# Performance work log

Hardware: AMD Instinct MI355X
Metric: run time of the kernel (lower is better)

The kernel has to match this reference:

```python
import jax, jax.numpy as jnp
import numpy as np

B, T, D, R = 8, 2048, 2048, 4


def setup_inputs() -> dict:
    key = jax.random.key(0)
    ks = jax.random.split(key, 9)
    u = jax.random.normal(ks[0], (B, T, D), dtype=jnp.float32)
    # a chosen so tanh(a) ~ 0.995: keeps cumprod over T=2048 away from underflow
    a = 3.0 + 0.2 * jax.random.uniform(ks[1], (D,), dtype=jnp.float32)
    b = 0.02 * jax.random.normal(ks[2], (D,), dtype=jnp.float32)
    c = 0.02 * jax.random.normal(ks[3], (D,), dtype=jnp.float32)
    d = 0.02 * jax.random.normal(ks[4], (D,), dtype=jnp.float32)
    gate_w = jax.random.normal(ks[5], (D, D), dtype=jnp.float32) / np.float32(np.sqrt(D))
    gate_b = jnp.zeros((D,), dtype=jnp.float32)
    d_lr_u = 0.02 * jax.random.normal(ks[6], (D, R), dtype=jnp.float32)
    d_lr_v = 0.02 * jax.random.normal(ks[7], (R, D), dtype=jnp.float32)
    return {"u": u, "a": a, "b": b, "c": c, "d": d,
            "gate_w": gate_w, "gate_b": gate_b,
            "d_lr_u": d_lr_u, "d_lr_v": d_lr_v}


def reference(u, a, b, c, d, gate_w, gate_b, d_lr_u, d_lr_v):
    # u: [B,T,D]
    Bs, Ts, Ds = u.shape
    rank = d_lr_u.shape[1]
    # gated input (torch Linear: x @ W.T + bias)
    g = jax.nn.sigmoid(jnp.einsum('btd,ed->bte', u, gate_w) + gate_b)
    u_g = u * g
    aa = jnp.tanh(a)                                   # [D], in (-1,1)
    # low-rank correction to feedthrough d
    u_mean = jnp.mean(u_g, axis=1, keepdims=True)      # [B,1,D]
    d_lr = (u_mean @ d_lr_u) @ d_lr_v / max(1.0, float(rank))
    d_eff = d + d_lr                                   # [B,1,D]
    # diagonal SSM via cumprod/cumsum (G[t] = aa^(t+1)); per-channel, T-independent of B
    G = jnp.cumprod(jnp.broadcast_to(aa, (Ts, Ds)), axis=0)  # [T,D]
    bu = b * u_g                                       # [B,T,D]
    G_safe = G.at[0].set(jnp.maximum(G[0], 1e-6))
    z = bu / G_safe                                    # [B,T,D]
    s = G * jnp.cumsum(z, axis=1)                      # [B,T,D]
    y = c * s + d_eff * u_g
    return y
```

## Files before the change

kernel.cpp:

```cpp
#include <hip/hip_runtime.h>
#include <hip/hip_bf16.h>
#include <math.h>

#define Bq 8
#define Tq 2048
#define Dq 2048
#define Rq 4
#define Mq (Bq*Tq)
#define NC 16
#define CL (Tq/NC)

typedef __attribute__((ext_vector_type(8))) short bf16x8;
typedef __attribute__((ext_vector_type(4))) float f32x4;
typedef __attribute__((ext_vector_type(4))) unsigned short us4;
typedef __attribute__((ext_vector_type(8))) unsigned short us8;

__device__ __forceinline__ unsigned short f2bf(float x) {
    unsigned int u = __float_as_uint(x);
    unsigned int r = (u + 0x7fffu + ((u >> 16) & 1u)) >> 16;
    return (unsigned short)r;
}
__device__ __forceinline__ float bf2f(unsigned short h) {
    return __uint_as_float((unsigned)h << 16);
}

template<int UGBF>
__device__ __forceinline__ f32x4 ld4(const void* p, long long off) {
    if constexpr (UGBF) {
        us4 v = *(const us4*)((const unsigned short*)p + off);
        f32x4 r;
        r.x = bf2f(v.x); r.y = bf2f(v.y); r.z = bf2f(v.z); r.w = bf2f(v.w);
        return r;
    } else {
        return *(const f32x4*)((const float*)p + off);
    }
}

__global__ __launch_bounds__(256) void k0_convert(
    const float* __restrict__ u, const float* __restrict__ gw,
    const float* __restrict__ a,
    unsigned short* __restrict__ ubf, unsigned short* __restrict__ wbf,
    float* __restrict__ aat, float* __restrict__ aaLt,
    float* __restrict__ aapow)
{
    const long long uN4 = (long long)Mq * Dq / 4;
    const long long wN4 = (long long)Dq * Dq / 4;
    long long gid = (long long)blockIdx.x * blockDim.x + threadIdx.x;
    if (gid < Dq) {
        float aa = tanhf(a[gid]);
        aat[gid] = aa;
        aaLt[gid] = exp2f((float)CL * log2f(aa));
        float p = 1.0f;
        for (int k = 0; k <= 16; ++k) { aapow[k * Dq + gid] = p; p *= aa; }
    }
    long long stride = (long long)gridDim.x * blockDim.x;
    for (long long i = gid; i < uN4 + wN4; i += stride) {
        const float4* src; unsigned short* dst; long long j;
        if (i < uN4) { src = (const float4*)u;  dst = ubf; j = i; }
        else         { src = (const float4*)gw; dst = wbf; j = i - uN4; }
        float4 v = src[j];
        us4 p;
        p.x = f2bf(v.x); p.y = f2bf(v.y); p.z = f2bf(v.z); p.w = f2bf(v.w);
        *(us4*)(dst + j * 4) = p;
    }
}


#define PH_BAR __builtin_amdgcn_s_barrier()
#define PRIO1  __builtin_amdgcn_s_setprio(1)
#define PRIO0  __builtin_amdgcn_s_setprio(0)

#define LDA(K0, K1, qb) do { _Pragma("unroll") for (int f_ = 0; f_ < 4; ++f_) { \
    aF[0][f_] = *(const bf16x8*)&lds[(K0) + ((qb) + f_) * 1024]; \
    aF[1][f_] = *(const bf16x8*)&lds[(K1) + ((qb) + f_) * 1024]; } } while (0)

#define LDB(K0, K1, fnb) do { _Pragma("unroll") for (int f_ = 0; f_ < 2; ++f_) { \
    bF[0][(fnb) + f_] = *(const bf16x8*)&lds[(K0) + ((fnb) + f_) * 1024]; \
    bF[1][(fnb) + f_] = *(const bf16x8*)&lds[(K1) + ((fnb) + f_) * 1024]; } } while (0)

#define MMA(fmb, fnb) do { _Pragma("unroll") for (int ks_ = 0; ks_ < 2; ++ks_) \
    _Pragma("unroll") for (int fm_ = 0; fm_ < 4; ++fm_) \
    _Pragma("unroll") for (int fn_ = 0; fn_ < 2; ++fn_) \
        acc[(fmb) + fm_][(fnb) + fn_] = __builtin_amdgcn_mfma_f32_16x16x32_bf16( \
            aF[ks_][fm_], bF[ks_][(fnb) + fn_], acc[(fmb) + fm_][(fnb) + fn_], 0, 0, 0); } while (0)

#define GLD(P, DST) __builtin_amdgcn_global_load_lds( \
    (const __attribute__((address_space(1))) void*)(P), \
    (__attribute__((address_space(3))) void*)&lds[DST], 16, 0, 0)

#define STAGE4(P00, P01, P10, P11, DBASE, KOFF) do { \
    GLD((P00) + (KOFF), (DBASE));              \
    GLD((P01) + (KOFF), (DBASE) + 512);        \
    GLD((P10) + (KOFF), (DBASE) + 8192);       \
    GLD((P11) + (KOFF), (DBASE) + 8192 + 512); } while (0)

template<int UGBF>
__global__ __launch_bounds__(512, 2) void k1_gemm(
    const unsigned short* __restrict__ Abf,
    const unsigned short* __restrict__ Bbf,
    const float* __restrict__ gate_b,
    const float* __restrict__ bvec,
    const float* __restrict__ aapow,
    float* __restrict__ psum,
    float* __restrict__ carry,
    void* __restrict__ ug_)
{
    __shared__ unsigned short lds[65536];
    const int tid  = threadIdx.x;
    const int wave = tid >> 6, lane = tid & 63;
    const int wr = wave >> 2, wc = wave & 3;

    const int bid = blockIdx.x;
    const int swz = (bid & 7) * 64 + (bid >> 3);
    const int tm = (swz >> 3) * 256;
    const int tn = (swz & 7) * 256;

    const int rr = lane & 15, kq = lane >> 4;
    const int r7 = rr & 7;
    const int kb0 = (kq ^ r7) * 8;
    const int kb1 = ((4 + kq) ^ r7) * 8;

    const int aB = wr * 8192 + rr * 64;
    const int bB = 16384 + (wc >> 1) * 8192 + (wc & 1) * 4096 + rr * 64;
    const int swA0k0 = aB + kb0,          swA0k1 = aB + kb1;
    const int swA1k0 = aB + 32768 + kb0,  swA1k1 = aB + 32768 + kb1;
    const int swB0k0 = bB + kb0,          swB0k1 = bB + kb1;
    const int swB1k0 = bB + 32768 + kb0,  swB1k1 = bB + 32768 + kb1;

    const int grow  = lane >> 3;
    const int gslot = ((lane & 7) ^ grow) * 8;
    const unsigned short* gA00 = Abf + (long long)(tm + wave * 16 + grow) * Dq + gslot;
    const unsigned short* gA01 = gA00 + 8 * Dq;
    const unsigned short* gA10 = gA00 + 128 * Dq;
    const unsigned short* gA11 = gA00 + 136 * Dq;
    const unsigned short* gB00 = Bbf + (long long)(tn + wave * 16 + grow) * Dq + gslot;
    const unsigned short* gB01 = gB00 + 8 * Dq;
    const unsigned short* gB10 = gB00 + 128 * Dq;
    const unsigned short* gB11 = gB00 + 136 * Dq;

    f32x4 acc[8][4] = {};
    bf16x8 aF[2][4], bF[2][4];

    const int dA0 = wave * 1024;
    const int dB0 = 16384 + wave * 1024;

    STAGE4(gB00, gB01, gB10, gB11, dB0,         0);
    STAGE4(gA00, gA01, gA10, gA11, dA0,         0);
    STAGE4(gB00, gB01, gB10, gB11, dB0 + 32768, 64);
    STAGE4(gA00, gA01, gA10, gA11, dA0 + 32768, 64);
    asm volatile("s_waitcnt vmcnt(8)" ::: "memory");
    PH_BAR;

    const int NIT = Dq / 128;
    for (int it = 0; it < NIT; ++it) {
        const bool pre = (it < NIT - 1);

        LDA(swA0k0, swA0k1, 0); LDB(swB0k0, swB0k1, 0);
        PH_BAR; PRIO1; MMA(0, 0); PRIO0; PH_BAR;
        LDB(swB0k0, swB0k1, 2);
        PH_BAR; PRIO1; MMA(0, 2); PRIO0; PH_BAR;
        LDA(swA0k0, swA0k1, 4);
        if (pre) STAGE4(gB00, gB01, gB10, gB11, dB0, 128);
        PH_BAR; PRIO1; MMA(4, 0); PRIO0; PH_BAR;
        if (pre) STAGE4(gA00, gA01, gA10, gA11, dA0, 128);
        PH_BAR;
        if (pre) asm volatile("s_waitcnt vmcnt(8)" ::: "memory");
        else     asm volatile("s_waitcnt vmcnt(0)" ::: "memory");
        PRIO1; MMA(4, 2); PRIO0; PH_BAR;

        LDA(swA1k0, swA1k1, 0); LDB(swB1k0, swB1k1, 0);
        PH_BAR; PRIO1; MMA(0, 0); PRIO0; PH_BAR;
        LDB(swB1k0, swB1k1, 2);
        PH_BAR; PRIO1; MMA(0, 2); PRIO0; PH_BAR;
        LDA(swA1k0, swA1k1, 4);
        if (pre) STAGE4(gB00, gB01, gB10, gB11, dB0 + 32768, 192);
        PH_BAR; PRIO1; MMA(4, 0); PRIO0; PH_BAR;
        if (pre) STAGE4(gA00, gA01, gA10, gA11, dA0 + 32768, 192);
        PH_BAR;
        if (pre) asm volatile("s_waitcnt vmcnt(8)" ::: "memory");
        else     asm volatile("s_waitcnt vmcnt(0)" ::: "memory");
        PRIO1; MMA(4, 2); PRIO0; PH_BAR;

        gA00 += 128; gA01 += 128; gA10 += 128; gA11 += 128;
        gB00 += 128; gB01 += 128; gB10 += 128; gB11 += 128;
    }

#pragma unroll
    for (int fn = 0; fn < 4; ++fn) {
        const int col = wc * 64 + fn * 16 + rr;
        const float gb = gate_b[tn + col];
#pragma unroll
        for (int fm = 0; fm < 8; ++fm) {
#pragma unroll
            for (int j = 0; j < 4; ++j) {
                const int row = wr * 128 + fm * 16 + kq * 4 + j;
                const float logit = acc[fm][fn][j] + gb;
                const float sg = 1.0f / (1.0f + __expf(-logit));
                lds[row * 256 + (col ^ (kq << 4))] = f2bf(sg);
            }
        }
    }
    __syncthreads();

    const int lr2  = lane >> 5;
    const int cb32 = lane & 31;
    const int c0   = cb32 * 8;
    const int baseT = wave * 2 + lr2;
    const int cX = ((baseT >> 2) & 3) << 4;

    float bw[8], a16[8], w15[8];
    {
        const float* bp   = bvec + tn + c0;
        const float* a16p = aapow + 16 * Dq + tn + c0;
        const float* w15p = aapow + (15 - baseT) * Dq + tn + c0;
#pragma unroll
        for (int k = 0; k < 8; ++k) { bw[k] = bp[k]; a16[k] = a16p[k]; w15[k] = w15p[k]; }
    }

    float ps[2][8] = {}, cr[2][8] = {};
#pragma unroll
    for (int i = 0; i < 16; ++i) {
        const int r = baseT + i * 16;
        const int ck = i >> 3;
        const long long gidx = (long long)(tm + r) * Dq + tn + c0;
        const bf16x8 u8 = *(const bf16x8*)&Abf[gidx];
        const bf16x8 s8 = *(const bf16x8*)&lds[r * 256 + (c0 ^ cX)];
        float ug[8];
#pragma unroll
        for (int k = 0; k < 8; ++k) {
            ug[k] = bf2f((unsigned short)u8[k]) * bf2f((unsigned short)s8[k]);
            ps[ck][k] += ug[k];
            cr[ck][k] = a16[k] * cr[ck][k] + bw[k] * ug[k];
        }
        if constexpr (UGBF) {
            us8 o;
#pragma unroll
            for (int k = 0; k < 8; ++k) o[k] = f2bf(ug[k]);
            *(us8*)&((unsigned short*)ug_)[gidx] = o;
        } else {
            f32x4 o0, o1;
            o0.x = ug[0]; o0.y = ug[1]; o0.z = ug[2]; o0.w = ug[3];
            o1.x = ug[4]; o1.y = ug[5]; o1.z = ug[6]; o1.w = ug[7];
            *(f32x4*)&((float*)ug_)[gidx]     = o0;
            *(f32x4*)&((float*)ug_)[gidx + 4] = o1;
        }
    }
    __syncthreads();

    float* redf = (float*)lds;
    const int slot = (baseT + cb32) & 15;
#pragma unroll
    for (int ck = 0; ck < 2; ++ck)
#pragma unroll
        for (int k = 0; k < 8; ++k) {
            const int col = c0 + k;
            redf[((ck * 2 + 0) * 256 + col) * 16 + slot] = ps[ck][k];
            redf[((ck * 2 + 1) * 256 + col) * 16 + slot] = cr[ck][k] * w15[k];
        }
    __syncthreads();

    const int bb  = tm >> 11;
    const int ckb = (tm & 2047) >> 7;
#pragma unroll
    for (int ii = 0; ii < 2; ++ii) {
        const int item = tid + ii * 512;
        const int p = item >> 8, col = item & 255;
        const int ck = p >> 1, isC = p & 1;
        const int rot = (item & 3) * 4;
        float s = 0.f;
#pragma unroll
        for (int q = 0; q < 4; ++q) {
            const f32x4 v = *(const f32x4*)&redf[item * 16 + ((rot + q * 4) & 15)];
            s += v.x + v.y + v.z + v.w;
        }
        const long long gi = (long long)(bb * NC + ckb + ck) * Dq + tn + col;
        if (isC) carry[gi] = s; else psum[gi] = s;
    }
}

__global__ __launch_bounds__(256) void k3_deff(
    const float* __restrict__ psum, const float* __restrict__ dvec,
    const float* __restrict__ dlru, const float* __restrict__ dlrv,
    float* __restrict__ deff)
{
    const int bb = blockIdx.x, tid = threadIdx.x;
    __shared__ float red[4][256];
    __shared__ float proj[4];
    float pr[4] = {0.f, 0.f, 0.f, 0.f};
    for (int i = 0; i < Dq / 256; ++i) {
        int dd = tid + i * 256;
        float m = 0.f;
        for (int k = 0; k < NC; ++k) m += psum[((long long)bb * NC + k) * Dq + dd];
        m *= (1.0f / (float)Tq);
#pragma unroll
        for (int r = 0; r < 4; ++r) pr[r] += m * dlru[dd * Rq + r];
    }
#pragma unroll
    for (int r = 0; r < 4; ++r) red[r][tid] = pr[r];
    __syncthreads();
    for (int off = 128; off > 0; off >>= 1) {
        if (tid < off)
#pragma unroll
            for (int r = 0; r < 4; ++r) red[r][tid] += red[r][tid + off];
        __syncthreads();
    }
    if (tid < 4) proj[tid] = red[tid][0] * 0.25f;
    __syncthreads();
    float p0 = proj[0], p1 = proj[1], p2 = proj[2], p3 = proj[3];
    for (int i = 0; i < Dq / 256; ++i) {
        int e = tid + i * 256;
        float v = dvec[e] + p0 * dlrv[0 * Dq + e] + p1 * dlrv[1 * Dq + e]
                          + p2 * dlrv[2 * Dq + e] + p3 * dlrv[3 * Dq + e];
        deff[(long long)bb * Dq + e] = v;
    }
}

template<int UGBF>
__global__ __launch_bounds__(128) void k4_scanC(
    const void* __restrict__ ug, float* __restrict__ yout,
    const float* __restrict__ aat, const float* __restrict__ aaLt,
    const float* __restrict__ bvec, const float* __restrict__ cvec,
    const float* __restrict__ deff, const float* __restrict__ carry)
{
    const int d0 = blockIdx.x * 512 + threadIdx.x * 4;
    const int ck = blockIdx.y, bb = blockIdx.z;
    f32x4 aa  = *(const f32x4*)&aat[d0];
    f32x4 aaL = *(const f32x4*)&aaLt[d0];
    f32x4 bv  = *(const f32x4*)&bvec[d0];
    f32x4 cv  = *(const f32x4*)&cvec[d0];
    f32x4 de  = *(const f32x4*)&deff[(long long)bb * Dq + d0];
    f32x4 s = {0.f, 0.f, 0.f, 0.f};
    for (int j = 0; j < ck; ++j) {
        f32x4 cj = *(const f32x4*)&carry[((long long)bb * NC + j) * Dq + d0];
        s = aaL * s + cj;
    }
    const long long base = ((long long)bb * Tq + (long long)ck * CL) * Dq + d0;
    for (int t = 0; t < CL; ++t) {
        f32x4 x = ld4<UGBF>(ug, base + (long long)t * Dq);
        s = aa * s + bv * x;
        f32x4 y = cv * s + de * x;
        *(f32x4*)&yout[base + (long long)t * Dq] = y;
    }
}

extern "C" void kernel_launch(void* const* d_in, const int* in_sizes, int n_in,
                              void* d_out, int out_size, void* d_ws, size_t ws_size,
                              hipStream_t stream)
{
    const float* u    = (const float*)d_in[0];
    const float* a    = (const float*)d_in[1];
    const float* b    = (const float*)d_in[2];
    const float* c    = (const float*)d_in[3];
    const float* d    = (const float*)d_in[4];
    const float* gw   = (const float*)d_in[5];
    const float* gb   = (const float*)d_in[6];
    const float* dlru = (const float*)d_in[7];
    const float* dlrv = (const float*)d_in[8];
    float* out = (float*)d_out;

    char* ws = (char*)d_ws;
    const size_t sz_ubf = (size_t)Mq * Dq * 2;
    const size_t sz_wbf = (size_t)Dq * Dq * 2;
    const size_t sz_ug  = (size_t)Mq * Dq * 2;
    const size_t sz_ps  = (size_t)Bq * NC * Dq * 4;

    unsigned short* ubf = (unsigned short*)ws;
    unsigned short* wbf = (unsigned short*)(ws + sz_ubf);

    const size_t tail_sz = 2 * sz_ps + (size_t)Bq * Dq * 4
                         + 2 * (size_t)Dq * 4 + (size_t)17 * Dq * 4;
    const size_t need_bf16 = sz_ubf + sz_wbf + sz_ug + tail_sz;
    const bool ugbf_mode = (ws_size >= need_bf16);

    char* rest = ws + sz_ubf + sz_wbf;
    unsigned short* ugbf = (unsigned short*)rest;
    char* tail = ugbf_mode ? (rest + sz_ug) : rest;
    float* psum  = (float*)tail;
    float* carry = psum  + (size_t)Bq * NC * Dq;
    float* deff  = carry + (size_t)Bq * NC * Dq;
    float* aat   = deff  + (size_t)Bq * Dq;
    float* aaLt  = aat   + Dq;
    float* aapow = aaLt  + Dq;

    k0_convert<<<2048, 256, 0, stream>>>(u, gw, a, ubf, wbf, aat, aaLt, aapow);

    dim3 g2(Dq / 512, NC, Bq);
    if (ugbf_mode) {
        k1_gemm<1><<<512, 512, 0, stream>>>(ubf, wbf, gb, b, aapow, psum, carry, ugbf);
        k3_deff<<<Bq, 256, 0, stream>>>(psum, d, dlru, dlrv, deff);
        k4_scanC<1><<<g2, 128, 0, stream>>>(ugbf, out, aat, aaLt, b, c, deff, carry);
    } else {
        k1_gemm<0><<<512, 512, 0, stream>>>(ubf, wbf, gb, b, aapow, psum, carry, out);
        k3_deff<<<Bq, 256, 0, stream>>>(psum, d, dlru, dlrv, deff);
        k4_scanC<0><<<g2, 128, 0, stream>>>(out, out, aat, aaLt, b, c, deff, carry);
    }
}
```

Measured before the change: 238.3 us.

## Spread global-to-LDS prefetches across MMA phases in half-size chunks

Splits each four-load staging group into two-load chunks and interleaves them between the MMA phases of the GEMM main loop. A-tile prefetches for the next buffer are issued right after that buffer's fragments are read, and vmcnt/lgkmcnt waits are tightened to match. The aim is a steadier memory pipeline with less stall at the end of each half-iteration. It risks subtle LDS read/write hazards: the else branch in the second half has no wait, and buffer reuse ordering depends on exact counter arithmetic.

New measurement: 234.3 us, median of 3. About the same (-1.7%).

```diff
diff --git a/kernel.cpp b/kernel.cpp
--- a/kernel.cpp
+++ b/kernel.cpp
@@ -88,11 +88,9 @@
     (const __attribute__((address_space(1))) void*)(P), \
     (__attribute__((address_space(3))) void*)&lds[DST], 16, 0, 0)
 
-#define STAGE4(P00, P01, P10, P11, DBASE, KOFF) do { \
-    GLD((P00) + (KOFF), (DBASE));              \
-    GLD((P01) + (KOFF), (DBASE) + 512);        \
-    GLD((P10) + (KOFF), (DBASE) + 8192);       \
-    GLD((P11) + (KOFF), (DBASE) + 8192 + 512); } while (0)
+#define STAGE2(P0, P1, DBASE, KOFF) do { \
+    GLD((P0) + (KOFF), (DBASE));         \
+    GLD((P1) + (KOFF), (DBASE) + 512); } while (0)
 
 template<int UGBF>
 __global__ __launch_bounds__(512, 2) void k1_gemm(
@@ -144,11 +142,13 @@
     const int dA0 = wave * 1024;
     const int dB0 = 16384 + wave * 1024;
 
-    STAGE4(gB00, gB01, gB10, gB11, dB0,         0);
-    STAGE4(gA00, gA01, gA10, gA11, dA0,         0);
-    STAGE4(gB00, gB01, gB10, gB11, dB0 + 32768, 64);
-    STAGE4(gA00, gA01, gA10, gA11, dA0 + 32768, 64);
-    asm volatile("s_waitcnt vmcnt(8)" ::: "memory");
+    STAGE2(gA00, gA01, dA0,                0);
+    STAGE2(gA10, gA11, dA0 + 8192,         0);
+    STAGE2(gB00, gB01, dB0,                0);
+    STAGE2(gB10, gB11, dB0 + 8192,         0);
+    STAGE2(gB00, gB01, dB0 + 32768,        64);
+    STAGE2(gB10, gB11, dB0 + 32768 + 8192, 64);
+    asm volatile("s_waitcnt vmcnt(4)" ::: "memory");
     PH_BAR;
 
     const int NIT = Dq / 128;
@@ -156,30 +156,44 @@
         const bool pre = (it < NIT - 1);
 
         LDA(swA0k0, swA0k1, 0); LDB(swB0k0, swB0k1, 0);
+        STAGE2(gA00, gA01, dA0 + 32768, 64);
+        asm volatile("s_waitcnt lgkmcnt(8)" ::: "memory");
         PH_BAR; PRIO1; MMA(0, 0); PRIO0; PH_BAR;
+
         LDB(swB0k0, swB0k1, 2);
+        STAGE2(gA10, gA11, dA0 + 32768 + 8192, 64);
         PH_BAR; PRIO1; MMA(0, 2); PRIO0; PH_BAR;
+
         LDA(swA0k0, swA0k1, 4);
-        if (pre) STAGE4(gB00, gB01, gB10, gB11, dB0, 128);
+        if (pre) STAGE2(gB00, gB01, dB0, 128);
         PH_BAR; PRIO1; MMA(4, 0); PRIO0; PH_BAR;
-        if (pre) STAGE4(gA00, gA01, gA10, gA11, dA0, 128);
-        PH_BAR;
-        if (pre) asm volatile("s_waitcnt vmcnt(8)" ::: "memory");
-        else     asm volatile("s_waitcnt vmcnt(0)" ::: "memory");
-        PRIO1; MMA(4, 2); PRIO0; PH_BAR;
+
+        if (pre) {
+            STAGE2(gB10, gB11, dB0 + 8192, 128);
+            asm volatile("s_waitcnt vmcnt(4)" ::: "memory");
+        } else {
+            asm volatile("s_waitcnt vmcnt(0)" ::: "memory");
+        }
+        PH_BAR; PRIO1; MMA(4, 2); PRIO0; PH_BAR;
 
         LDA(swA1k0, swA1k1, 0); LDB(swB1k0, swB1k1, 0);
+        if (pre) STAGE2(gA00, gA01, dA0, 128);
+        asm volatile("s_waitcnt lgkmcnt(8)" ::: "memory");
         PH_BAR; PRIO1; MMA(0, 0); PRIO0; PH_BAR;
+
         LDB(swB1k0, swB1k1, 2);
+        if (pre) STAGE2(gA10, gA11, dA0 + 8192, 128);
         PH_BAR; PRIO1; MMA(0, 2); PRIO0; PH_BAR;
+
         LDA(swA1k0, swA1k1, 4);
-        if (pre) STAGE4(gB00, gB01, gB10, gB11, dB0 + 32768, 192);
+        if (pre) STAGE2(gB00, gB01, dB0 + 32768, 192);
         PH_BAR; PRIO1; MMA(4, 0); PRIO0; PH_BAR;
-        if (pre) STAGE4(gA00, gA01, gA10, gA11, dA0 + 32768, 192);
-        PH_BAR;
-        if (pre) asm volatile("s_waitcnt vmcnt(8)" ::: "memory");
-        else     asm volatile("s_waitcnt vmcnt(0)" ::: "memory");
-        PRIO1; MMA(4, 2); PRIO0; PH_BAR;
+
+        if (pre) {
+            STAGE2(gB10, gB11, dB0 + 32768 + 8192, 192);
+            asm volatile("s_waitcnt vmcnt(4)" ::: "memory");
+        }
+        PH_BAR; PRIO1; MMA(4, 2); PRIO0; PH_BAR;
 
         gA00 += 128; gA01 += 128; gA10 += 128; gA11 += 128;
         gB00 += 128; gB01 += 128; gB10 += 128; gB11 += 128;
```
